# Performance work log

Hardware: AMD Instinct MI355X
Metric: run time of the kernel (lower is better)

Reference implementation:

```python
import jax, jax.numpy as jnp
import numpy as np

L, B, S, D, N, H = 4, 4, 1024, 1024, 64, 16   # layers, batch, seq, d_model, d_state, heads
DI = 2 * D      # d_inner (expand_factor=2)
DH = D // H     # head dim
DF = 4 * D      # ffn hidden
SCALE = 1.0 / np.sqrt(DH)


def setup_inputs() -> dict:
    key = jax.random.key(0)
    ks = jax.random.split(key, 12)
    w = lambda k, sh: jax.random.normal(k, sh, jnp.float32) * 0.02
    return {
        "x": jax.random.normal(ks[0], (B, S, D), jnp.float32),
        "A_log": jax.random.normal(ks[1], (L, N), jnp.float32),
        "Dp": jax.random.normal(ks[2], (L, D), jnp.float32),
        "W_in": w(ks[3], (L, 2 * DI, D)), "b_in": jnp.zeros((L, 2 * DI), jnp.float32),
        "W_xp": w(ks[4], (L, N, DI)), "b_xp": jnp.zeros((L, N), jnp.float32),
        "W_dt": w(ks[5], (L, D, DI)), "b_dt": jnp.zeros((L, D), jnp.float32),
        "W_out": w(ks[6], (L, D, DI)), "b_out": jnp.zeros((L, D), jnp.float32),
        "W_qkv": w(ks[7], (L, 3 * D, D)), "b_qkv": jnp.zeros((L, 3 * D), jnp.float32),
        "W_ao": w(ks[8], (L, D, D)), "b_ao": jnp.zeros((L, D), jnp.float32),
        "g1": jnp.ones((L, D), jnp.float32), "be1": jnp.zeros((L, D), jnp.float32),
        "g2": jnp.ones((L, D), jnp.float32), "be2": jnp.zeros((L, D), jnp.float32),
        "W_f1": w(ks[9], (L, DF, D)), "b_f1": jnp.zeros((L, DF), jnp.float32),
        "W_f2": w(ks[10], (L, D, DF)), "b_f2": jnp.zeros((L, D), jnp.float32),
    }


def _ln(x, g, b, eps=1e-5):
    mu = x.mean(-1, keepdims=True)
    var = ((x - mu) ** 2).mean(-1, keepdims=True)
    return (x - mu) * jax.lax.rsqrt(var + eps) * g + b


def _mamba(x, A_log, Dp, W_in, b_in, W_xp, b_xp, W_dt, b_dt, W_out, b_out):
    xr = jnp.einsum('bsd,od->bso', x, W_in) + b_in          # [b,s,2*DI]
    xi, res = jnp.split(xr, 2, axis=-1)
    xi = jax.nn.silu(xi)
    A = -jnp.exp(A_log)                                      # [N]
    delta = jax.nn.softplus(jnp.einsum('bsi,di->bsd', xi, W_dt) + b_dt)  # [b,s,D]
    m = delta.mean(-1)                                       # [b,s]
    A_disc = jnp.exp(A[None, None, :] * m[:, :, None])       # [b,s,N]
    u = jnp.einsum('bsi,ni->bsn', xi, W_xp) + b_xp           # [b,s,N]

    def step(state, inp):
        a_t, u_t = inp
        state = a_t * state + u_t                            # [b,N]
        return state, state.sum(-1)                          # carry, emit sum over d_state

    init = jnp.zeros((x.shape[0], A_log.shape[0]), x.dtype)
    _, ssum = jax.lax.scan(step, init, (A_disc.swapaxes(0, 1), u.swapaxes(0, 1)))
    ssum = ssum.swapaxes(0, 1)                               # [b,s]
    y = ssum[..., None] * xi                                 # [b,s,DI]
    y = y * jax.nn.silu(res)
    y = jnp.einsum('bsi,di->bsd', y, W_out) + b_out
    return y + x * Dp


def _attn(x, W_qkv, b_qkv, W_ao, b_ao):
    b, s, d = x.shape
    qkv = jnp.einsum('bsd,od->bso', x, W_qkv) + b_qkv        # [b,s,3d]
    qkv = qkv.reshape(b, s, 3, H, DH)
    q = jnp.moveaxis(qkv[:, :, 0], 2, 1)                     # [b,h,s,dh]
    k = jnp.moveaxis(qkv[:, :, 1], 2, 1)
    v = jnp.moveaxis(qkv[:, :, 2], 2, 1)
    scores = jnp.einsum('bhqd,bhkd->bhqk', q, k) * SCALE
    wts = jax.nn.softmax(scores, axis=-1)
    o = jnp.einsum('bhqk,bhkd->bhqd', wts, v)
    o = jnp.moveaxis(o, 1, 2).reshape(b, s, d)
    return jnp.einsum('bsd,od->bso', o, W_ao) + b_ao


def _forward(x, A_log, Dp, W_in, b_in, W_xp, b_xp, W_dt, b_dt, W_out, b_out,
             W_qkv, b_qkv, W_ao, b_ao, g1, be1, g2, be2, W_f1, b_f1, W_f2, b_f2):
    for l in range(L):
        m = _mamba(x, A_log[l], Dp[l], W_in[l], b_in[l], W_xp[l], b_xp[l],
                   W_dt[l], b_dt[l], W_out[l], b_out[l])
        x = _ln(x + m, g1[l], be1[l])
        a = _attn(x, W_qkv[l], b_qkv[l], W_ao[l], b_ao[l])
        x = _ln(x + a, g2[l], be2[l])
        h = jax.nn.gelu(jnp.einsum('bsd,fd->bsf', x, W_f1[l]) + b_f1[l], approximate=False)
        x = x + jnp.einsum('bsf,df->bsd', h, W_f2[l]) + b_f2[l]
    return x


def reference(x, A_log, Dp, W_in, b_in, W_xp, b_xp, W_dt, b_dt, W_out, b_out,
              W_qkv, b_qkv, W_ao, b_ao, g1, be1, g2, be2, W_f1, b_f1, W_f2, b_f2):
    return _forward(x, A_log, Dp, W_in, b_in, W_xp, b_xp, W_dt, b_dt, W_out, b_out,
                    W_qkv, b_qkv, W_ao, b_ao, g1, be1, g2, be2, W_f1, b_f1, W_f2, b_f2)
```

## Files before the change

kernel.cpp:

```cpp
#include <hip/hip_runtime.h>
#include <math.h>

typedef unsigned short ushort_t;
typedef unsigned int uint_t;
typedef __attribute__((ext_vector_type(8))) short short8;
typedef __attribute__((ext_vector_type(4))) float f32x4;

constexpr int Bb = 4, Ss = 1024, Dd = 1024, Nn = 64, Hh = 16;
constexpr int DIi = 2048, DFf = 4096;
constexpr int TOKENS = Bb * Ss;

constexpr size_t O_IN  = 0;
constexpr size_t O_DT  = 4194304;
constexpr size_t O_XP  = O_DT + 2097152;
constexpr size_t O_OUT = O_XP + 262144;
constexpr size_t O_QKV = O_OUT + 2097152;
constexpr size_t O_AO  = O_QKV + 3145728;
constexpr size_t O_F1  = O_AO + 1048576;
constexpr size_t O_F2  = O_F1 + 4194304;
constexpr size_t W_TOTAL = O_F2 + 4194304;
constexpr size_t W_QUADS = W_TOTAL / 4;

enum { EPI_SPLIT = 0, EPI_B16, EPI_GELU, EPI_DTXP, EPI_DP, EPI_F32, EPI_RESID };

__device__ __forceinline__ float siluf(float x) { return x / (1.f + expf(-x)); }
__device__ __forceinline__ float softplusf(float x) { return fmaxf(x, 0.f) + log1pf(expf(-fabsf(x))); }
__device__ __forceinline__ float geluf(float x) { return 0.5f * x * (1.f + erff(x * 0.7071067811865476f)); }

__device__ __forceinline__ float bf2f(uint_t u) {
    union { uint_t i; float f; } v; v.i = u << 16; return v.f;
}
__device__ __forceinline__ ushort_t f2bf(float f) {
    union { float f; uint_t i; } v; v.f = f;
    return (ushort_t)((v.i + 0x7FFFu + ((v.i >> 16) & 1u)) >> 16);
}

__device__ __forceinline__ void gload_lds16(const ushort_t* g, ushort_t* l) {
    __builtin_amdgcn_global_load_lds(
        (const __attribute__((address_space(1))) unsigned int*)g,
        (__attribute__((address_space(3))) unsigned int*)l, 16, 0, 0);
}

__device__ __forceinline__ void wait_vm(int n) {
    if (n == 0)      asm volatile("s_waitcnt vmcnt(0)" ::: "memory");
    else if (n == 3) asm volatile("s_waitcnt vmcnt(3)" ::: "memory");
    else if (n == 4) asm volatile("s_waitcnt vmcnt(4)" ::: "memory");
    else if (n == 6) asm volatile("s_waitcnt vmcnt(6)" ::: "memory");
    else             asm volatile("s_waitcnt vmcnt(8)" ::: "memory");
}

template <int EPI, int MT, int NBUF, int XBY>
__global__ __launch_bounds__(256) void gemm_mfma(
    const ushort_t* __restrict__ A, const ushort_t* __restrict__ Bw,
    const float* __restrict__ bias, int M, int N, int K,
    float* __restrict__ of0, float* __restrict__ of1,
    ushort_t* __restrict__ ob0, ushort_t* __restrict__ ob1,
    const float* __restrict__ e0, const float* __restrict__ e1)
{
    constexpr int BUFSZ = (MT == 128) ? 8192 : 6144;
    constexpr int DEPTH = NBUF - 1;
    constexpr int L     = (MT == 128) ? 4 : 3;
    constexpr int NJ    = (MT == 128) ? 4 : 2;
    constexpr int XBX   = 8 / XBY;
    __shared__ __attribute__((aligned(16))) ushort_t AB[NBUF * BUFSZ];

    const int tid = threadIdx.x;
    const int lane = tid & 63, wid = tid >> 6;
    const int wr = (MT == 128) ? (wid >> 1) : 0;
    const int wc = (MT == 128) ? (wid & 1) : wid;
    const int l15 = lane & 15, lg = lane >> 4;

    int bx = blockIdx.x, by = blockIdx.y;
    const int gx = gridDim.x, gy = gridDim.y;
    if ((gy % XBY) == 0 && (gx % XBX) == 0) {
        const int s = by * gx + bx;
        const int xcd = s & 7, c = s >> 3;
        const int gyc = gy / XBY, gxc = gx / XBX;
        by = (xcd % XBY) * gyc + (c % gyc);
        bx = (xcd / XBY) * gxc + (c / gyc);
    }
    const int m0 = by * MT, n0 = bx << 7;

    f32x4 acc[4][NJ];
#pragma unroll
    for (int i = 0; i < 4; ++i)
#pragma unroll
        for (int j = 0; j < NJ; ++j) { acc[i][j][0] = 0.f; acc[i][j][1] = 0.f; acc[i][j][2] = 0.f; acc[i][j][3] = 0.f; }

    const int srow4 = lane >> 2;
    const int scc4  = (lane & 3) ^ ((lane >> 3) & 3);
    const ushort_t* Ag = A + (size_t)(m0 + wid * 32 + srow4) * K + scc4 * 8;
    const ushort_t* Bg = Bw + (size_t)(n0 + wid * 32 + srow4) * K + scc4 * 8;
    const ushort_t* sb64[3];
    int do64[3];
    if (MT == 64) {
#pragma unroll
        for (int j = 0; j < 3; ++j) {
            const int i = wid * 3 + j;
            const bool isA = i < 4;
            const int rb = (isA ? i : i - 4) * 16;
            sb64[j] = (isA ? A + (size_t)(m0 + rb + srow4) * K
                           : Bw + (size_t)(n0 + rb + srow4) * K) + scc4 * 8;
            do64[j] = (isA ? 0 : 2048) + rb * 32;
        }
    }

    auto STAGE = [&](int b_, int k0_) {
        ushort_t* d_ = AB + b_ * BUFSZ;
        if constexpr (MT == 128) {
            gload_lds16(Ag + k0_,                  d_ + (wid * 32) * 32);
            gload_lds16(Ag + (size_t)16 * K + k0_, d_ + (wid * 32 + 16) * 32);
            gload_lds16(Bg + k0_,                  d_ + 4096 + (wid * 32) * 32);
            gload_lds16(Bg + (size_t)16 * K + k0_, d_ + 4096 + (wid * 32 + 16) * 32);
        } else {
#pragma unroll
            for (int j = 0; j < 3; ++j)
                gload_lds16(sb64[j] + k0_, d_ + do64[j]);
        }
    };

    const int NS = K >> 5;
#pragma unroll
    for (int p = 0; p < DEPTH; ++p) STAGE(p, p * 32);
    wait_vm((DEPTH - 1) * L);
    __builtin_amdgcn_s_barrier();

    const int chAB = (lg ^ ((l15 >> 1) & 3)) * 8;
    int bc = 0, bp = DEPTH;
    for (int s = 0; s < NS; ++s) {
        if (s + DEPTH < NS) STAGE(bp, (s + DEPTH) << 5);
        const ushort_t* As_ = AB + bc * BUFSZ;
        const ushort_t* Bs_ = As_ + ((MT == 128) ? 4096 : 2048);
        short8 af[4], bfr[NJ];
#pragma unroll
        for (int mi = 0; mi < 4; ++mi)
            af[mi] = *(const short8*)&As_[(wr * 64 + mi * 16 + l15) * 32 + chAB];
#pragma unroll
        for (int nj = 0; nj < NJ; ++nj)
            bfr[nj] = *(const short8*)&Bs_[(wc * (MT == 128 ? 64 : 32) + nj * 16 + l15) * 32 + chAB];
#pragma unroll
        for (int mi = 0; mi < 4; ++mi)
#pragma unroll
            for (int nj = 0; nj < NJ; ++nj)
                acc[mi][nj] = __builtin_amdgcn_mfma_f32_16x16x32_bf16(
                    af[mi], bfr[nj], acc[mi][nj], 0, 0, 0);
        if (s + 1 < NS) {
            const int rem = NS - 2 - s;
            wait_vm(((rem < DEPTH - 1) ? rem : DEPTH - 1) * L);
            __builtin_amdgcn_s_barrier();
        }
        bc = (bc + 1 == NBUF) ? 0 : bc + 1;
        bp = (bp + 1 == NBUF) ? 0 : bp + 1;
    }
    __syncthreads();

    if constexpr (MT == 128) {
        const bool lo = (EPI != EPI_SPLIT) || (n0 < DIi);
#pragma unroll
        for (int nj = 0; nj < 4; ++nj) {
            const int coll = wc * 64 + nj * 16 + l15;
            const float bv = bias[n0 + coll];
#pragma unroll
            for (int mi = 0; mi < 4; ++mi)
#pragma unroll
                for (int r = 0; r < 4; ++r) {
                    float v = acc[mi][nj][r] + bv;
                    if (EPI == EPI_SPLIT) v = lo ? siluf(v) : v;
                    else if (EPI == EPI_GELU) v = geluf(v);
                    AB[(wr * 64 + mi * 16 + lg * 4 + r) * 128 + coll] = f2bf(v);
                }
        }
        __syncthreads();
        ushort_t* dst = (EPI == EPI_SPLIT) ? (lo ? ob0 : ob1) : ob0;
        const int Nd = (EPI == EPI_SPLIT) ? DIi : N;
        const int nb = (EPI == EPI_SPLIT && !lo) ? (n0 - DIi) : n0;
#pragma unroll
        for (int i = 0; i < 8; ++i) {
            const int c = i * 256 + tid;
            const int row = c >> 4, ch = c & 15;
            *(uint4*)&dst[(size_t)(m0 + row) * Nd + nb + ch * 8] =
                *(const uint4*)&AB[row * 128 + ch * 8];
        }
    } else {
        float* Cf = (float*)AB;
#pragma unroll
        for (int nj = 0; nj < NJ; ++nj) {
            const int coll = wc * 32 + nj * 16 + l15;
            const float bv = bias[n0 + coll];
#pragma unroll
            for (int mi = 0; mi < 4; ++mi)
#pragma unroll
                for (int r = 0; r < 4; ++r)
                    Cf[(mi * 16 + lg * 4 + r) * 128 + coll] = acc[mi][nj][r] + bv;
        }
        __syncthreads();
#pragma unroll
        for (int i = 0; i < 8; ++i) {
            const int c = i * 256 + tid;
            const int row = c >> 5, ch = c & 31;
            const int grow = m0 + row;
            const int gcol = n0 + ch * 4;
            float4 v = *(const float4*)&Cf[row * 128 + ch * 4];
            if (EPI == EPI_DTXP) {
                if (n0 < Dd) {
                    v.x = softplusf(v.x); v.y = softplusf(v.y);
                    v.z = softplusf(v.z); v.w = softplusf(v.w);
                    *(float4*)&of0[(size_t)grow * Dd + gcol] = v;
                } else {
                    *(float4*)&of1[(size_t)grow * 128 + (gcol - Dd)] = v;
                }
            } else if (EPI == EPI_DP) {
                const float4 e = *(const float4*)&e0[(size_t)grow * N + gcol];
                const float4 d = *(const float4*)&e1[gcol];
                v.x = fmaf(e.x, d.x, v.x); v.y = fmaf(e.y, d.y, v.y);
                v.z = fmaf(e.z, d.z, v.z); v.w = fmaf(e.w, d.w, v.w);
                *(float4*)&of0[(size_t)grow * N + gcol] = v;
            } else if (EPI == EPI_F32) {
                *(float4*)&of0[(size_t)grow * N + gcol] = v;
            } else {
                const float4 e = *(const float4*)&e0[(size_t)grow * N + gcol];
                v.x += e.x; v.y += e.y; v.z += e.z; v.w += e.w;
                *(float4*)&of0[(size_t)grow * N + gcol] = v;
                uint2 w;
                w.x = (uint_t)f2bf(v.x) | ((uint_t)f2bf(v.y) << 16);
                w.y = (uint_t)f2bf(v.z) | ((uint_t)f2bf(v.w) << 16);
                *(uint2*)&ob0[(size_t)grow * N + gcol] = w;
            }
        }
    }
}

__global__ __launch_bounds__(256) void convert_weights_kernel(
    const float* __restrict__ Win, const float* __restrict__ Wdt,
    const float* __restrict__ Wxp, const float* __restrict__ Wout,
    const float* __restrict__ Wqkv, const float* __restrict__ Wao,
    const float* __restrict__ Wf1, const float* __restrict__ Wf2,
    const float* __restrict__ bdt, const float* __restrict__ bxp,
    ushort_t* __restrict__ dst, float* __restrict__ bcat)
{
    size_t q = (size_t)blockIdx.x * blockDim.x + threadIdx.x;
    if (q < 288) {
#pragma unroll
        for (int j = 0; j < 4; ++j) {
            const int e = (int)q * 4 + j;
            bcat[e] = (e < Dd) ? bdt[e] : ((e < Dd + Nn) ? bxp[e - Dd] : 0.f);
        }
    }
    const size_t stride = (size_t)gridDim.x * blockDim.x;
    for (; q < W_QUADS; q += stride) {
        const size_t e = q * 4;
        float4 v;
        if (e < O_DT)       v = *(const float4*)&Win[e - O_IN];
        else if (e < O_XP)  v = *(const float4*)&Wdt[e - O_DT];
        else if (e < O_OUT) {
            const size_t li = e - O_XP;
            const int row = (int)(li >> 11), colq = (int)(li & 2047);
            v = (row < Nn) ? *(const float4*)&Wxp[(size_t)row * DIi + colq]
                           : make_float4(0.f, 0.f, 0.f, 0.f);
        }
        else if (e < O_QKV) v = *(const float4*)&Wout[e - O_OUT];
        else if (e < O_AO)  v = *(const float4*)&Wqkv[e - O_QKV];
        else if (e < O_F1)  v = *(const float4*)&Wao[e - O_AO];
        else if (e < O_F2)  v = *(const float4*)&Wf1[e - O_F1];
        else                v = *(const float4*)&Wf2[e - O_F2];
        uint2 w;
        w.x = (uint_t)f2bf(v.x) | ((uint_t)f2bf(v.y) << 16);
        w.y = (uint_t)f2bf(v.z) | ((uint_t)f2bf(v.w) << 16);
        *(uint2*)&dst[e] = w;
    }
}

__global__ __launch_bounds__(256) void cvt_f32_bf16_kernel(
    const float* __restrict__ in, ushort_t* __restrict__ out)
{
    const size_t i4 = (size_t)blockIdx.x * blockDim.x + threadIdx.x;
    const float4 v = *(const float4*)&in[i4 * 4];
    uint2 w;
    w.x = (uint_t)f2bf(v.x) | ((uint_t)f2bf(v.y) << 16);
    w.y = (uint_t)f2bf(v.z) | ((uint_t)f2bf(v.w) << 16);
    *(uint2*)&out[i4 * 4] = w;
}

__global__ __launch_bounds__(256) void row_mean_kernel(const float* __restrict__ in,
                                                       float* __restrict__ out)
{
    __shared__ float red[4];
    const int tid = threadIdx.x;
    const size_t base = (size_t)blockIdx.x * Dd;
    const float4 v = *(const float4*)&in[base + tid * 4];
    float s = v.x + v.y + v.z + v.w;
#pragma unroll
    for (int off = 32; off; off >>= 1) s += __shfl_xor(s, off);
    if ((tid & 63) == 0) red[tid >> 6] = s;
    __syncthreads();
    if (tid == 0) out[blockIdx.x] = (red[0] + red[1] + red[2] + red[3]) * (1.f / (float)Dd);
}

__global__ __launch_bounds__(256) void ln_residual_kernel(
    float* __restrict__ xio, const float* __restrict__ addin,
    const float* __restrict__ g, const float* __restrict__ be,
    ushort_t* __restrict__ xb)
{
    __shared__ float red[8];
    const int tid = threadIdx.x;
    const size_t base = (size_t)blockIdx.x * Dd;
    const float4 xv = *(const float4*)&xio[base + tid * 4];
    const float4 av = *(const float4*)&addin[base + tid * 4];
    float v[4] = {xv.x + av.x, xv.y + av.y, xv.z + av.z, xv.w + av.w};
    float s = v[0] + v[1] + v[2] + v[3];
    float s2 = v[0] * v[0] + v[1] * v[1] + v[2] * v[2] + v[3] * v[3];
#pragma unroll
    for (int off = 32; off; off >>= 1) { s += __shfl_xor(s, off); s2 += __shfl_xor(s2, off); }
    if ((tid & 63) == 0) { red[tid >> 6] = s; red[4 + (tid >> 6)] = s2; }
    __syncthreads();
    const float mu = (red[0] + red[1] + red[2] + red[3]) * (1.f / (float)Dd);
    const float var = (red[4] + red[5] + red[6] + red[7]) * (1.f / (float)Dd) - mu * mu;
    const float rstd = rsqrtf(var + 1e-5f);
    const float4 gv = *(const float4*)&g[tid * 4];
    const float4 bv = *(const float4*)&be[tid * 4];
    float o[4];
    o[0] = (v[0] - mu) * rstd * gv.x + bv.x;
    o[1] = (v[1] - mu) * rstd * gv.y + bv.y;
    o[2] = (v[2] - mu) * rstd * gv.z + bv.z;
    o[3] = (v[3] - mu) * rstd * gv.w + bv.w;
    *(float4*)&xio[base + tid * 4] = make_float4(o[0], o[1], o[2], o[3]);
    uint2 w;
    w.x = (uint_t)f2bf(o[0]) | ((uint_t)f2bf(o[1]) << 16);
    w.y = (uint_t)f2bf(o[2]) | ((uint_t)f2bf(o[3]) << 16);
    *(uint2*)&xb[base + tid * 4] = w;
}

__global__ __launch_bounds__(1024) void scan_fused_kernel(
    const float* __restrict__ A_log_l, const float* __restrict__ m,
    const float* __restrict__ u, float* __restrict__ ssum)
{
    __shared__ float Ps[16][64];
    __shared__ float Sl[16][64];
    __shared__ float Cs[16][64];
    const int b = blockIdx.x;
    const int tid = threadIdx.x;
    const int n = tid & 63, c = tid >> 6;
    const int t0 = b * Ss + c * 64;
    const float Aval = -expf(A_log_l[n]);

    float S = 0.f, msum = 0.f;
#pragma unroll 8
    for (int t = 0; t < 64; ++t) {
        const float mt = m[t0 + t];
        msum += mt;
        S = fmaf(expf(Aval * mt), S, u[(size_t)(t0 + t) * 128 + n]);
    }
    Ps[c][n] = expf(Aval * msum);
    Sl[c][n] = S;
    __syncthreads();

    if (c == 0) {
        float carry = 0.f;
#pragma unroll
        for (int cc = 0; cc < 16; ++cc) {
            Cs[cc][n] = carry;
            carry = fmaf(Ps[cc][n], carry, Sl[cc][n]);
        }
    }
    __syncthreads();

    float st = Cs[c][n];
#pragma unroll 4
    for (int t = 0; t < 64; ++t) {
        st = fmaf(expf(Aval * m[t0 + t]), st, u[(size_t)(t0 + t) * 128 + n]);
        float r = st;
#pragma unroll
        for (int off = 32; off; off >>= 1) r += __shfl_xor(r, off);
        if (n == 0) ssum[t0 + t] = r;
    }
}

__global__ __launch_bounds__(256) void y_gate_kernel(
    ushort_t* __restrict__ xi, const ushort_t* __restrict__ res,
    const float* __restrict__ ssum)
{
    const size_t i8 = (size_t)blockIdx.x * blockDim.x + threadIdx.x;
    const int t = (int)(i8 >> 8);
    const float sv = ssum[t];
    uint4 xw = *(const uint4*)&xi[i8 * 8];
    const uint4 rw = *(const uint4*)&res[i8 * 8];
    const uint_t xs[4] = {xw.x, xw.y, xw.z, xw.w};
    const uint_t rs[4] = {rw.x, rw.y, rw.z, rw.w};
    uint_t os[4];
#pragma unroll
    for (int j = 0; j < 4; ++j) {
        const float x0 = bf2f(xs[j] & 0xffffu), x1 = bf2f(xs[j] >> 16);
        const float r0 = bf2f(rs[j] & 0xffffu), r1 = bf2f(rs[j] >> 16);
        os[j] = (uint_t)f2bf(sv * x0 * siluf(r0)) | ((uint_t)f2bf(sv * x1 * siluf(r1)) << 16);
    }
    *(uint4*)&xi[i8 * 8] = make_uint4(os[0], os[1], os[2], os[3]);
}

__global__ __launch_bounds__(256) void transpose_v_kernel(
    const ushort_t* __restrict__ qkv, ushort_t* __restrict__ vt)
{
    __shared__ ushort_t T[64][68];
    const int b = blockIdx.z, h = blockIdx.y, st = blockIdx.x;
    const int tid = threadIdx.x;
    const int sl = tid >> 3, d0 = (tid & 7) * 8;
#pragma unroll
    for (int it = 0; it < 2; ++it) {
        const int s = sl + it * 32;
        const uint4 w = *(const uint4*)&qkv[(size_t)(b * Ss + st * 64 + s) * 3072 + 2048 + h * 64 + d0];
        *(uint2*)&T[s][d0]     = make_uint2(w.x, w.y);
        *(uint2*)&T[s][d0 + 4] = make_uint2(w.z, w.w);
    }
    __syncthreads();
    const int dl = tid >> 3, s0 = (tid & 7) * 8;
#pragma unroll
    for (int it = 0; it < 2; ++it) {
        const int d = dl + it * 32;
        uint_t w[4];
#pragma unroll
        for (int j = 0; j < 4; ++j)
            w[j] = (uint_t)T[s0 + 2 * j][d] | ((uint_t)T[s0 + 2 * j + 1][d] << 16);
        *(uint4*)&vt[(size_t)((b * Hh + h) * 64 + d) * Ss + st * 64 + s0] =
            make_uint4(w[0], w[1], w[2], w[3]);
    }
}

__global__ __launch_bounds__(256) void attn_mfma_kernel(
    const ushort_t* __restrict__ qkv, const ushort_t* __restrict__ vt,
    ushort_t* __restrict__ out)
{
    __shared__ ushort_t Ks[64 * 64];
    __shared__ ushort_t Vs[64 * 64];
    __shared__ __attribute__((aligned(16))) ushort_t Pb[4][2560];

    const int tid = threadIdx.x;
    const int lane = tid & 63, wid = tid >> 6;
    const int b = blockIdx.z, h = blockIdx.y;
    const int q0 = blockIdx.x * 128 + wid * 32;
    const int l15 = lane & 15, lg = lane >> 4;
    constexpr float CEXP = 0.125f * 1.44269504f;

    short8 qf[2][2];
#pragma unroll
    for (int mi = 0; mi < 2; ++mi)
#pragma unroll
        for (int kk = 0; kk < 2; ++kk)
            qf[mi][kk] = *(const short8*)&qkv[(size_t)(b * Ss + q0 + mi * 16 + l15) * 3072
                                              + h * 64 + kk * 32 + lg * 8];

    f32x4 oacc[2][4];
#pragma unroll
    for (int mi = 0; mi < 2; ++mi)
#pragma unroll
        for (int nj = 0; nj < 4; ++nj) { oacc[mi][nj][0]=0.f; oacc[mi][nj][1]=0.f; oacc[mi][nj][2]=0.f; oacc[mi][nj][3]=0.f; }
    float lrun[2][4];
#pragma unroll
    for (int mi = 0; mi < 2; ++mi)
#pragma unroll
        for (int r = 0; r < 4; ++r) lrun[mi][r] = 0.f;

    const int srow = lane >> 3;
    const int scc  = (lane & 7) ^ srow;
    const ushort_t* Kg = qkv + (size_t)(b * Ss + wid * 16 + srow) * 3072 + 1024 + h * 64 + scc * 8;
    const ushort_t* Vg = vt + (size_t)((b * Hh + h) * 64 + wid * 16 + srow) * Ss + scc * 8;

    for (int kt = 0; kt < Ss / 64; ++kt) {
#pragma unroll
        for (int j = 0; j < 2; ++j) {
            gload_lds16(Kg + (size_t)(kt * 64 + j * 8) * 3072, Ks + (wid * 16 + j * 8) * 64);
            gload_lds16(Vg + (size_t)j * 8 * Ss + kt * 64,     Vs + (wid * 16 + j * 8) * 64);
        }
        __syncthreads();

        f32x4 sacc[2][4];
#pragma unroll
        for (int mi = 0; mi < 2; ++mi)
#pragma unroll
            for (int nj = 0; nj < 4; ++nj) { sacc[mi][nj][0]=0.f; sacc[mi][nj][1]=0.f; sacc[mi][nj][2]=0.f; sacc[mi][nj][3]=0.f; }
#pragma unroll
        for (int kk = 0; kk < 2; ++kk) {
            short8 kf[4];
#pragma unroll
            for (int nj = 0; nj < 4; ++nj) {
                const int row = nj * 16 + l15;
                const int ch = (kk * 4 + lg) ^ (row & 7);
                kf[nj] = *(const short8*)&Ks[row * 64 + ch * 8];
            }
#pragma unroll
            for (int mi = 0; mi < 2; ++mi)
#pragma unroll
                for (int nj = 0; nj < 4; ++nj)
                    sacc[mi][nj] = __builtin_amdgcn_mfma_f32_16x16x32_bf16(
                        qf[mi][kk], kf[nj], sacc[mi][nj], 0, 0, 0);
        }

#pragma unroll
        for (int mi = 0; mi < 2; ++mi)
#pragma unroll
            for (int nj = 0; nj < 4; ++nj) {
                const int bi = mi * 2 + (nj >> 1);
                const int chsw = ((nj & 1) * 2 + (l15 >> 3)) ^ lg;
#pragma unroll
                for (int r = 0; r < 4; ++r) {
                    const float p = exp2f(sacc[mi][nj][r] * CEXP);
                    lrun[mi][r] += p;
                    const int q15 = lg * 4 + r;
                    Pb[wid][bi * 640 + q15 * 40 + chsw * 8 + (lane & 7)] = f2bf(p);
                }
            }

#pragma unroll
        for (int kk = 0; kk < 2; ++kk) {
            short8 pa[2], vb[4];
#pragma unroll
            for (int mi = 0; mi < 2; ++mi) {
                const int chsw = lg ^ (l15 >> 2);
                pa[mi] = *(const short8*)&Pb[wid][(mi * 2 + kk) * 640 + l15 * 40 + chsw * 8];
            }
#pragma unroll
            for (int nj = 0; nj < 4; ++nj) {
                const int row = nj * 16 + l15;
                const int ch = (kk * 4 + lg) ^ (row & 7);
                vb[nj] = *(const short8*)&Vs[row * 64 + ch * 8];
            }
#pragma unroll
            for (int mi = 0; mi < 2; ++mi)
#pragma unroll
                for (int nj = 0; nj < 4; ++nj)
                    oacc[mi][nj] = __builtin_amdgcn_mfma_f32_16x16x32_bf16(
                        pa[mi], vb[nj], oacc[mi][nj], 0, 0, 0);
        }
        __syncthreads();
    }

#pragma unroll
    for (int mi = 0; mi < 2; ++mi)
#pragma unroll
        for (int r = 0; r < 4; ++r) {
            float s = lrun[mi][r];
#pragma unroll
            for (int off = 1; off < 16; off <<= 1) s += __shfl_xor(s, off);
            lrun[mi][r] = 1.f / s;
        }
#pragma unroll
    for (int mi = 0; mi < 2; ++mi)
#pragma unroll
        for (int r = 0; r < 4; ++r) {
            const int q = q0 + mi * 16 + lg * 4 + r;
            const float inv = lrun[mi][r];
#pragma unroll
            for (int nj = 0; nj < 4; ++nj)
                out[(size_t)(b * Ss + q) * Dd + h * 64 + nj * 16 + l15] =
                    f2bf(oacc[mi][nj][r] * inv);
        }
}

extern "C" void kernel_launch(void* const* d_in, const int* in_sizes, int n_in,
                              void* d_out, int out_size, void* d_ws, size_t ws_size,
                              hipStream_t stream)
{
    const float* x_in  = (const float*)d_in[0];
    const float* A_log = (const float*)d_in[1];
    const float* Dp    = (const float*)d_in[2];
    const float* W_in  = (const float*)d_in[3];
    const float* b_in  = (const float*)d_in[4];
    const float* W_xp  = (const float*)d_in[5];
    const float* b_xp  = (const float*)d_in[6];
    const float* W_dt  = (const float*)d_in[7];
    const float* b_dt  = (const float*)d_in[8];
    const float* W_out = (const float*)d_in[9];
    const float* b_out = (const float*)d_in[10];
    const float* W_qkv = (const float*)d_in[11];
    const float* b_qkv = (const float*)d_in[12];
    const float* W_ao  = (const float*)d_in[13];
    const float* b_ao  = (const float*)d_in[14];
    const float* g1    = (const float*)d_in[15];
    const float* be1   = (const float*)d_in[16];
    const float* g2    = (const float*)d_in[17];
    const float* be2   = (const float*)d_in[18];
    const float* W_f1  = (const float*)d_in[19];
    const float* b_f1  = (const float*)d_in[20];
    const float* W_f2  = (const float*)d_in[21];
    const float* b_f2  = (const float*)d_in[22];

    float* xf      = (float*)d_ws;
    float* a3      = xf + 4194304;
    float* ub      = a3 + 4194304;
    float* mb      = ub + 524288;
    float* sb      = mb + 4096;
    float* bcat    = sb + 4096;
    ushort_t* xb    = (ushort_t*)(bcat + 1152);
    ushort_t* xi_b  = xb + 4194304;
    ushort_t* res_b = xi_b + 8388608;
    ushort_t* qh_b  = res_b + 8388608;
    ushort_t* ao_b  = qh_b + 16777216;
    ushort_t* Wb    = ao_b + 4194304;
    ushort_t* vt_b  = Wb + W_TOTAL;

    hipMemcpyAsync(xf, x_in, (size_t)TOKENS * Dd * sizeof(float),
                   hipMemcpyDeviceToDevice, stream);
    cvt_f32_bf16_kernel<<<dim3(4096), dim3(256), 0, stream>>>(x_in, xb);

    const dim3 blk(256);

    for (int l = 0; l < 4; ++l) {
        convert_weights_kernel<<<dim3(2048), blk, 0, stream>>>(
            W_in + (size_t)l * 4194304, W_dt + (size_t)l * 2097152,
            W_xp + (size_t)l * 131072,  W_out + (size_t)l * 2097152,
            W_qkv + (size_t)l * 3145728, W_ao + (size_t)l * 1048576,
            W_f1 + (size_t)l * 4194304, W_f2 + (size_t)l * 4194304,
            b_dt + (size_t)l * 1024, b_xp + (size_t)l * Nn, Wb, bcat);

        gemm_mfma<EPI_SPLIT, 128, 4, 4><<<dim3(32, 32), blk, 0, stream>>>(
            xb, Wb + O_IN, b_in + (size_t)l * 4096, TOKENS, 4096, 1024,
            nullptr, nullptr, xi_b, res_b, nullptr, nullptr);
        gemm_mfma<EPI_DTXP, 64, 4, 8><<<dim3(9, 64), blk, 0, stream>>>(
            xi_b, Wb + O_DT, bcat, TOKENS, 1152, 2048,
            a3, ub, nullptr, nullptr, nullptr, nullptr);
        row_mean_kernel<<<dim3(TOKENS), blk, 0, stream>>>(a3, mb);
        scan_fused_kernel<<<dim3(Bb), dim3(1024), 0, stream>>>(
            A_log + (size_t)l * Nn, mb, ub, sb);
        y_gate_kernel<<<dim3(4096), blk, 0, stream>>>(xi_b, res_b, sb);
        gemm_mfma<EPI_DP, 64, 4, 8><<<dim3(8, 64), blk, 0, stream>>>(
            xi_b, Wb + O_OUT, b_out + (size_t)l * 1024, TOKENS, 1024, 2048,
            a3, nullptr, nullptr, nullptr, xf, Dp + (size_t)l * 1024);
        ln_residual_kernel<<<dim3(TOKENS), blk, 0, stream>>>(
            xf, a3, g1 + (size_t)l * 1024, be1 + (size_t)l * 1024, xb);
        gemm_mfma<EPI_B16, 128, 3, 4><<<dim3(24, 32), blk, 0, stream>>>(
            xb, Wb + O_QKV, b_qkv + (size_t)l * 3072, TOKENS, 3072, 1024,
            nullptr, nullptr, qh_b, nullptr, nullptr, nullptr);
        transpose_v_kernel<<<dim3(16, Hh, Bb), blk, 0, stream>>>(qh_b, vt_b);
        attn_mfma_kernel<<<dim3(8, Hh, Bb), blk, 0, stream>>>(qh_b, vt_b, ao_b);
        gemm_mfma<EPI_F32, 64, 4, 8><<<dim3(8, 64), blk, 0, stream>>>(
            ao_b, Wb + O_AO, b_ao + (size_t)l * 1024, TOKENS, 1024, 1024,
            a3, nullptr, nullptr, nullptr, nullptr, nullptr);
        ln_residual_kernel<<<dim3(TOKENS), blk, 0, stream>>>(
            xf, a3, g2 + (size_t)l * 1024, be2 + (size_t)l * 1024, xb);
        gemm_mfma<EPI_GELU, 128, 4, 4><<<dim3(32, 32), blk, 0, stream>>>(
            xb, Wb + O_F1, b_f1 + (size_t)l * 4096, TOKENS, 4096, 1024,
            nullptr, nullptr, qh_b, nullptr, nullptr, nullptr);
        gemm_mfma<EPI_RESID, 64, 4, 8><<<dim3(8, 64), blk, 0, stream>>>(
            qh_b, Wb + O_F2, b_f2 + (size_t)l * 1024, TOKENS, 1024, 4096,
            xf, nullptr, xb, nullptr, xf, nullptr);
    }

    hipMemcpyAsync(d_out, xf, (size_t)TOKENS * Dd * sizeof(float),
                   hipMemcpyDeviceToDevice, stream);
    (void)in_sizes; (void)n_in; (void)out_size; (void)ws_size;
}
```

Before: 1.847 ms.

## Fuse delta row-mean into DTXP epilogue and V transpose into QKV epilogue

The DTXP GEMM epilogue now reduces softplus(delta) into per-128-column partial sums instead of writing the full delta matrix. The scan kernel sums these eight partials per token to get the mean, which removes row_mean_kernel and a large fp32 write and read. The QKV GEMM epilogue writes the V columns directly in transposed per-head layout, which removes transpose_v_kernel and its extra pass over V. The cost is strided narrow global stores in the QKV epilogue and extra shuffles in the DTXP epilogue.

New measurement: 1.819 ms. Within noise of the previous version (-1.5%).

```diff
diff --git a/kernel.cpp b/kernel.cpp
--- a/kernel.cpp
+++ b/kernel.cpp
@@ -21,7 +21,7 @@
 constexpr size_t W_TOTAL = O_F2 + 4194304;
 constexpr size_t W_QUADS = W_TOTAL / 4;
 
-enum { EPI_SPLIT = 0, EPI_B16, EPI_GELU, EPI_DTXP, EPI_DP, EPI_F32, EPI_RESID };
+enum { EPI_SPLIT = 0, EPI_QKV, EPI_GELU, EPI_DTXP, EPI_DP, EPI_F32, EPI_RESID };
 
 __device__ __forceinline__ float siluf(float x) { return x / (1.f + expf(-x)); }
 __device__ __forceinline__ float softplusf(float x) { return fmaxf(x, 0.f) + log1pf(expf(-fabsf(x))); }
@@ -171,15 +171,34 @@
                 }
         }
         __syncthreads();
-        ushort_t* dst = (EPI == EPI_SPLIT) ? (lo ? ob0 : ob1) : ob0;
-        const int Nd = (EPI == EPI_SPLIT) ? DIi : N;
-        const int nb = (EPI == EPI_SPLIT && !lo) ? (n0 - DIi) : n0;
-#pragma unroll
-        for (int i = 0; i < 8; ++i) {
-            const int c = i * 256 + tid;
-            const int row = c >> 4, ch = c & 15;
-            *(uint4*)&dst[(size_t)(m0 + row) * Nd + nb + ch * 8] =
-                *(const uint4*)&AB[row * 128 + ch * 8];
+        if (EPI == EPI_QKV && n0 >= 2048) {
+            const int bb = m0 >> 10, srow0 = m0 & 1023;
+#pragma unroll
+            for (int it = 0; it < 8; ++it) {
+                const int task = it * 256 + tid;
+                const int dim = task & 127;
+                const int strip = task >> 7;
+                uint_t w[4];
+#pragma unroll
+                for (int j = 0; j < 4; ++j) {
+                    const int s2 = strip * 8 + 2 * j;
+                    w[j] = (uint_t)AB[s2 * 128 + dim] | ((uint_t)AB[(s2 + 1) * 128 + dim] << 16);
+                }
+                const int vd = (n0 - 2048) + dim;
+                *(uint4*)&ob1[((size_t)(bb * Hh + (vd >> 6)) * 64 + (vd & 63)) * Ss + srow0 + strip * 8] =
+                    make_uint4(w[0], w[1], w[2], w[3]);
+            }
+        } else {
+            ushort_t* dst = (EPI == EPI_SPLIT) ? (lo ? ob0 : ob1) : ob0;
+            const int Nd = (EPI == EPI_SPLIT) ? DIi : N;
+            const int nb = (EPI == EPI_SPLIT && !lo) ? (n0 - DIi) : n0;
+#pragma unroll
+            for (int i = 0; i < 8; ++i) {
+                const int c = i * 256 + tid;
+                const int row = c >> 4, ch = c & 15;
+                *(uint4*)&dst[(size_t)(m0 + row) * Nd + nb + ch * 8] =
+                    *(const uint4*)&AB[row * 128 + ch * 8];
+            }
         }
     } else {
         float* Cf = (float*)AB;
@@ -203,9 +222,11 @@
             float4 v = *(const float4*)&Cf[row * 128 + ch * 4];
             if (EPI == EPI_DTXP) {
                 if (n0 < Dd) {
-                    v.x = softplusf(v.x); v.y = softplusf(v.y);
-                    v.z = softplusf(v.z); v.w = softplusf(v.w);
-                    *(float4*)&of0[(size_t)grow * Dd + gcol] = v;
+                    float ps = softplusf(v.x) + softplusf(v.y) + softplusf(v.z) + softplusf(v.w);
+#pragma unroll
+                    for (int off = 1; off < 32; off <<= 1) ps += __shfl_xor(ps, off);
+                    if ((lane & 31) == 0)
+                        of0[(size_t)grow * 8 + (n0 >> 7)] = ps;
                 } else {
                     *(float4*)&of1[(size_t)grow * 128 + (gcol - Dd)] = v;
                 }
@@ -281,21 +302,6 @@
     *(uint2*)&out[i4 * 4] = w;
 }
 
-__global__ __launch_bounds__(256) void row_mean_kernel(const float* __restrict__ in,
-                                                       float* __restrict__ out)
-{
-    __shared__ float red[4];
-    const int tid = threadIdx.x;
-    const size_t base = (size_t)blockIdx.x * Dd;
-    const float4 v = *(const float4*)&in[base + tid * 4];
-    float s = v.x + v.y + v.z + v.w;
-#pragma unroll
-    for (int off = 32; off; off >>= 1) s += __shfl_xor(s, off);
-    if ((tid & 63) == 0) red[tid >> 6] = s;
-    __syncthreads();
-    if (tid == 0) out[blockIdx.x] = (red[0] + red[1] + red[2] + red[3]) * (1.f / (float)Dd);
-}
-
 __global__ __launch_bounds__(256) void ln_residual_kernel(
     float* __restrict__ xio, const float* __restrict__ addin,
     const float* __restrict__ g, const float* __restrict__ be,
@@ -331,22 +337,32 @@
 }
 
 __global__ __launch_bounds__(1024) void scan_fused_kernel(
-    const float* __restrict__ A_log_l, const float* __restrict__ m,
+    const float* __restrict__ A_log_l, const float* __restrict__ part,
     const float* __restrict__ u, float* __restrict__ ssum)
 {
     __shared__ float Ps[16][64];
     __shared__ float Sl[16][64];
     __shared__ float Cs[16][64];
+    __shared__ float Ms[16][64];
     const int b = blockIdx.x;
     const int tid = threadIdx.x;
     const int n = tid & 63, c = tid >> 6;
     const int t0 = b * Ss + c * 64;
     const float Aval = -expf(A_log_l[n]);
 
+    {
+        const float* pp = part + (size_t)(t0 + n) * 8;
+        float ps = 0.f;
+#pragma unroll
+        for (int j = 0; j < 8; ++j) ps += pp[j];
+        Ms[c][n] = ps * (1.f / 1024.f);
+    }
+    __syncthreads();
+
     float S = 0.f, msum = 0.f;
 #pragma unroll 8
     for (int t = 0; t < 64; ++t) {
-        const float mt = m[t0 + t];
+        const float mt = Ms[c][t];
         msum += mt;
         S = fmaf(expf(Aval * mt), S, u[(size_t)(t0 + t) * 128 + n]);
     }
@@ -367,7 +383,7 @@
     float st = Cs[c][n];
 #pragma unroll 4
     for (int t = 0; t < 64; ++t) {
-        st = fmaf(expf(Aval * m[t0 + t]), st, u[(size_t)(t0 + t) * 128 + n]);
+        st = fmaf(expf(Aval * Ms[c][t]), st, u[(size_t)(t0 + t) * 128 + n]);
         float r = st;
 #pragma unroll
         for (int off = 32; off; off >>= 1) r += __shfl_xor(r, off);
@@ -394,34 +410,6 @@
         os[j] = (uint_t)f2bf(sv * x0 * siluf(r0)) | ((uint_t)f2bf(sv * x1 * siluf(r1)) << 16);
     }
     *(uint4*)&xi[i8 * 8] = make_uint4(os[0], os[1], os[2], os[3]);
-}
-
-__global__ __launch_bounds__(256) void transpose_v_kernel(
-    const ushort_t* __restrict__ qkv, ushort_t* __restrict__ vt)
-{
-    __shared__ ushort_t T[64][68];
-    const int b = blockIdx.z, h = blockIdx.y, st = blockIdx.x;
-    const int tid = threadIdx.x;
-    const int sl = tid >> 3, d0 = (tid & 7) * 8;
-#pragma unroll
-    for (int it = 0; it < 2; ++it) {
-        const int s = sl + it * 32;
-        const uint4 w = *(const uint4*)&qkv[(size_t)(b * Ss + st * 64 + s) * 3072 + 2048 + h * 64 + d0];
-        *(uint2*)&T[s][d0]     = make_uint2(w.x, w.y);
-        *(uint2*)&T[s][d0 + 4] = make_uint2(w.z, w.w);
-    }
-    __syncthreads();
-    const int dl = tid >> 3, s0 = (tid & 7) * 8;
-#pragma unroll
-    for (int it = 0; it < 2; ++it) {
-        const int d = dl + it * 32;
-        uint_t w[4];
-#pragma unroll
-        for (int j = 0; j < 4; ++j)
-            w[j] = (uint_t)T[s0 + 2 * j][d] | ((uint_t)T[s0 + 2 * j + 1][d] << 16);
-        *(uint4*)&vt[(size_t)((b * Hh + h) * 64 + d) * Ss + st * 64 + s0] =
-            make_uint4(w[0], w[1], w[2], w[3]);
-    }
 }
 
 __global__ __launch_bounds__(256) void attn_mfma_kernel(
@@ -585,9 +573,9 @@
     float* xf      = (float*)d_ws;
     float* a3      = xf + 4194304;
     float* ub      = a3 + 4194304;
-    float* mb      = ub + 524288;
-    float* sb      = mb + 4096;
-    float* bcat    = sb + 4096;
+    float* sb      = ub + 524288;
+    float* part    = sb + 4096;
+    float* bcat    = part + 32768;
     ushort_t* xb    = (ushort_t*)(bcat + 1152);
     ushort_t* xi_b  = xb + 4194304;
     ushort_t* res_b = xi_b + 8388608;
@@ -615,20 +603,18 @@
             nullptr, nullptr, xi_b, res_b, nullptr, nullptr);
         gemm_mfma<EPI_DTXP, 64, 4, 8><<<dim3(9, 64), blk, 0, stream>>>(
             xi_b, Wb + O_DT, bcat, TOKENS, 1152, 2048,
-            a3, ub, nullptr, nullptr, nullptr, nullptr);
-        row_mean_kernel<<<dim3(TOKENS), blk, 0, stream>>>(a3, mb);
+            part, ub, nullptr, nullptr, nullptr, nullptr);
         scan_fused_kernel<<<dim3(Bb), dim3(1024), 0, stream>>>(
-            A_log + (size_t)l * Nn, mb, ub, sb);
+            A_log + (size_t)l * Nn, part, ub, sb);
         y_gate_kernel<<<dim3(4096), blk, 0, stream>>>(xi_b, res_b, sb);
         gemm_mfma<EPI_DP, 64, 4, 8><<<dim3(8, 64), blk, 0, stream>>>(
             xi_b, Wb + O_OUT, b_out + (size_t)l * 1024, TOKENS, 1024, 2048,
             a3, nullptr, nullptr, nullptr, xf, Dp + (size_t)l * 1024);
         ln_residual_kernel<<<dim3(TOKENS), blk, 0, stream>>>(
             xf, a3, g1 + (size_t)l * 1024, be1 + (size_t)l * 1024, xb);
-        gemm_mfma<EPI_B16, 128, 3, 4><<<dim3(24, 32), blk, 0, stream>>>(
+        gemm_mfma<EPI_QKV, 128, 3, 4><<<dim3(24, 32), blk, 0, stream>>>(
             xb, Wb + O_QKV, b_qkv + (size_t)l * 3072, TOKENS, 3072, 1024,
-            nullptr, nullptr, qh_b, nullptr, nullptr, nullptr);
-        transpose_v_kernel<<<dim3(16, Hh, Bb), blk, 0, stream>>>(qh_b, vt_b);
+            nullptr, nullptr, qh_b, vt_b, nullptr, nullptr);
         attn_mfma_kernel<<<dim3(8, Hh, Bb), blk, 0, stream>>>(qh_b, vt_b, ao_b);
         gemm_mfma<EPI_F32, 64, 4, 8><<<dim3(8, 64), blk, 0, stream>>>(
             ao_b, Wb + O_AO, b_ao + (size_t)l * 1024, TOKENS, 1024, 1024,
```
